# Kernel tuning notes

Measured on AMD Instinct MI355X. Metric: run time of the kernel, lower is better.

Reference implementation:

```python
import jax, jax.numpy as jnp
import numpy as np

NUM_HEADS = 8
BLOCK = 8      # block_size
HALO = 2       # kernel_size (halo width)


def _rel_to_abs(rel):
    # halo-style relative->absolute conversion
    # rel: [B, G, qh, qw, 2*p-1] -> [B, G, qh, qw, p]
    B, G, qh, qw, dim = rel.shape
    p = (dim + 1) // 2
    gap = p - qw
    flat = rel.reshape(B, G, qh, qw * dim)[:, :, :, qw - 1:-1]
    return flat.reshape(B, G, qh, qw, 2 * (p - 1))[:, :, :, :, gap:p + gap]


def _relative_logits(pos_q, pos_emb_h, pos_emb_w):
    # pos_q: [B, G, qb, qb, kd]; pos_emb_*: [kd, 2*p-1]
    rel_w = _rel_to_abs(jnp.einsum('bghwd,dr->bghwr', pos_q, pos_emb_w))  # [B,G,qb,qb,p] key-width
    q_t = pos_q.transpose(0, 1, 3, 2, 4)
    rel_h = _rel_to_abs(jnp.einsum('bgwhd,dr->bgwhr', q_t, pos_emb_h))
    rel_h = rel_h.transpose(0, 1, 3, 2, 4)  # [B,G,qb,qb,p] key-height
    return rel_h[..., :, None] + rel_w[..., None, :]  # [B,G,qb,qb,p,p]


def reference(x, w_q, w_kv, w_out, pos_emb_h, pos_emb_w):
    B, H, W, C = x.shape
    kd = C // NUM_HEADS                # per-head key dim
    kvk = BLOCK + 2 * HALO             # halo window size
    out_ch = w_out.shape[1]
    v_dim = out_ch // NUM_HEADS
    kv_per_head = (C + out_ch) // NUM_HEADS
    hh, ww = H // BLOCK, W // BLOCK
    scale = float(1.0 / np.sqrt(kd))

    # ---- query (1x1 conv == matmul), blockify ----
    q = (x @ w_q).reshape(B, hh, BLOCK, ww, BLOCK, NUM_HEADS, kd)
    q = q.transpose(0, 5, 1, 3, 2, 4, 6)  # [B,nh,hh,ww,qb,qb,kd]
    attn_q = q.reshape(B, NUM_HEADS, hh, ww, BLOCK * BLOCK, kd) * scale
    pos_q = q.reshape(B, NUM_HEADS * hh * ww, BLOCK, BLOCK, kd)

    # ---- key/value: 1x1 conv, halo pad, unfold into overlapping windows ----
    kv = jnp.pad(x @ w_kv, ((0, 0), (HALO, HALO), (HALO, HALO), (0, 0)))
    idx = np.arange(hh)[:, None] * BLOCK + np.arange(kvk)[None, :]  # [hh,kvk]
    idy = np.arange(ww)[:, None] * BLOCK + np.arange(kvk)[None, :]  # [ww,kvk]
    patches = kv[:, idx][:, :, :, idy]           # [B,hh,kvk,ww,kvk,kv_dim]
    patches = patches.transpose(0, 1, 3, 2, 4, 5)  # [B,hh,ww,kvk,kvk,kv_dim]
    kvh = patches.reshape(B, hh, ww, kvk, kvk, NUM_HEADS, kv_per_head)
    kvh = kvh.transpose(0, 5, 1, 2, 3, 4, 6).reshape(B, NUM_HEADS, hh, ww, kvk * kvk, kv_per_head)
    key, value = kvh[..., :kd], kvh[..., kd:]

    # ---- attention with relative position bias ----
    scores = jnp.einsum('bnhwqd,bnhwkd->bnhwqk', attn_q, key)
    pos = _relative_logits(pos_q, pos_emb_h, pos_emb_w)
    pos = pos.reshape(B, NUM_HEADS, hh, ww, BLOCK * BLOCK, kvk * kvk)
    attn = jax.nn.softmax(scores + pos, axis=-1)
    out = jnp.einsum('bnhwqk,bnhwkv->bnhwqv', attn, value)  # [B,nh,hh,ww,qb*qb,v_dim]

    # ---- de-blockify, output projection ----
    out = out.reshape(B, NUM_HEADS, hh, ww, BLOCK, BLOCK, v_dim)
    out = out.transpose(0, 2, 4, 3, 5, 1, 6).reshape(B, H, W, NUM_HEADS * v_dim)
    return out @ w_out


def setup_inputs() -> dict:
    key = jax.random.key(0)
    ks = jax.random.split(key, 6)
    B, H, W, C = 4, 128, 128, 256
    out_ch = 256
    kd = C // NUM_HEADS
    kvk = BLOCK + 2 * HALO
    std = kd ** -0.5
    return {
        'x': jax.random.normal(ks[0], (B, H, W, C), jnp.float32),
        'w_q': jax.random.normal(ks[1], (C, C), jnp.float32) * 0.02,
        'w_kv': jax.random.normal(ks[2], (C, C + out_ch), jnp.float32) * 0.02,
        'w_out': jax.random.normal(ks[3], (C, out_ch), jnp.float32) * 0.02,
        'pos_emb_h': jax.random.normal(ks[4], (kd, 2 * kvk - 1), jnp.float32) * std,
        'pos_emb_w': jax.random.normal(ks[5], (kd, 2 * kvk - 1), jnp.float32) * std,
    }
```

## Files before the change

kernel.cpp:

```cpp
#include <hip/hip_runtime.h>
#include <hip/hip_bf16.h>
#include <cstdint>


#define KVK 12
#define NKEYS 144
#define VT_S 160
#define PT_S 168
#define LOG2E 1.4426950408889634f

typedef unsigned int u32;
typedef unsigned short u16;
typedef __attribute__((ext_vector_type(8))) __bf16 bf16x8;
typedef __attribute__((ext_vector_type(4))) float f32x4;

__device__ __forceinline__ u16 f2bf(float f) {
    u32 x = __float_as_uint(f);
    return (u16)((x + 0x7fffu + ((x >> 16) & 1u)) >> 16);
}
__device__ __forceinline__ u32 cvtpk(float lo, float hi) {
    u32 d;
    asm("v_cvt_pk_bf16_f32 %0, %1, %2" : "=v"(d) : "v"(lo), "v"(hi));
    return d;
}
__device__ __forceinline__ float max3f(float a, float b, float c) {
    float d;
    asm("v_max3_f32 %0, %1, %2, %3" : "=v"(d) : "v"(a), "v"(b), "v"(c));
    return d;
}
__device__ __forceinline__ float exp2a(float x) {
    float d;
    asm("v_exp_f32 %0, %1" : "=v"(d) : "v"(x));
    return d;
}
__device__ __forceinline__ void gload16(const void* g, void* l) {
    __builtin_amdgcn_global_load_lds(
        (const __attribute__((address_space(1))) void*)g,
        (__attribute__((address_space(3))) void*)l, 16, 0, 0);
}

__global__ __launch_bounds__(256) void prep_weights(const float* __restrict__ wq,
                                                    const float* __restrict__ wkv,
                                                    const float* __restrict__ wout,
                                                    u16* __restrict__ wT,
                                                    u16* __restrict__ woutT,
                                                    const float* __restrict__ emb_h,
                                                    const float* __restrict__ emb_w,
                                                    u16* __restrict__ embT) {
    int blk = blockIdx.x, t = threadIdx.x;
    if (blk < 256) {
        int idx = blk * 256 + t; int nn = idx >> 8, k = idx & 255;
        wT[idx] = f2bf(wq[(long)k * 256 + nn]);
    } else if (blk < 768) {
        int idx = (blk - 256) * 256 + t; int nn = idx >> 8, k = idx & 255;
        float v = wkv[(long)k * 512 + nn];
        if ((nn & 32) == 0) v *= 0.2550348642f;
        wT[65536 + idx] = f2bf(v);
    } else if (blk < 1024) {
        int idx = (blk - 768) * 256 + t; int nn = idx >> 8, k = idx & 255;
        woutT[idx] = f2bf(wout[(long)k * 256 + nn]);
    } else if (blk == 1024) {
        for (int i = t; i < 736; i += 256) {
            int p = i >> 5, d = i & 31;
            embT[i] = f2bf(emb_h[d * 23 + p]);
        }
    } else {
        for (int i = t; i < 736; i += 256) {
            int p = i >> 5, d = i & 31;
            embT[736 + i] = f2bf(emb_w[d * 23 + p]);
        }
    }
}

__global__ __launch_bounds__(256) void gemm_qkv(const float* __restrict__ X,
                                                const u16* __restrict__ WT,
                                                u16* __restrict__ Qb,
                                                u16* __restrict__ KVb) {
    __shared__ u16 Apan[128 * 256];
    __shared__ u16 Bs[4096];
    const int t = threadIdx.x;
    const int w = t >> 6, lane = t & 63;
    const long m0 = (long)blockIdx.x * 128;
    const int wr = w >> 1, wc = w & 1;
    const int r = lane & 15, g = lane >> 4;

    #pragma unroll
    for (int i = 0; i < 16; ++i) {
        int v = i * 256 + t;
        int row = v >> 5, u = v & 31;
        const float* src = X + (m0 + row) * 256 + u * 8;
        float4 f0 = *reinterpret_cast<const float4*>(src);
        float4 f1 = *reinterpret_cast<const float4*>(src + 4);
        uint4 pk;
        pk.x = cvtpk(f0.x, f0.y); pk.y = cvtpk(f0.z, f0.w);
        pk.z = cvtpk(f1.x, f1.y); pk.w = cvtpk(f1.z, f1.w);
        *reinterpret_cast<uint4*>(&Apan[row * 256 + ((u ^ (row & 7)) << 3)]) = pk;
    }

    const int u0 = w * 128 + lane;
    const int rowB0 = u0 >> 2, csB0 = (u0 & 3) * 8;
    const int u1 = u0 + 64;
    const int rowB1 = u1 >> 2, csB1 = (u1 & 3) * 8;
    u16* BsW = &Bs[w * 1024];

    for (int nt = 0; nt < 6; ++nt) {
        const long n0 = nt * 128;
        const u16* Bg0 = WT + (n0 + rowB0) * 256 + csB0;
        const u16* Bg1 = WT + (n0 + rowB1) * 256 + csB1;

        f32x4 acc[4][4];
        #pragma unroll
        for (int i = 0; i < 4; ++i)
            #pragma unroll
            for (int j = 0; j < 4; ++j) acc[i][j] = (f32x4){0.f, 0.f, 0.f, 0.f};

        for (int k0 = 0; k0 < 256; k0 += 32) {
            gload16(Bg0 + k0, BsW);
            gload16(Bg1 + k0, BsW + 512);
            __syncthreads();
            bf16x8 a[4], b[4];
            const int cu = k0 >> 3;
            #pragma unroll
            for (int i = 0; i < 4; ++i) {
                int row = wr * 64 + i * 16 + r;
                a[i] = *reinterpret_cast<const bf16x8*>(
                    &Apan[row * 256 + (((cu + g) ^ (row & 7)) << 3)]);
            }
            #pragma unroll
            for (int j = 0; j < 4; ++j)
                b[j] = *reinterpret_cast<const bf16x8*>(&Bs[(wc * 64 + j * 16 + r) * 32 + g * 8]);
            #pragma unroll
            for (int i = 0; i < 4; ++i)
                #pragma unroll
                for (int j = 0; j < 4; ++j)
                    acc[i][j] = __builtin_amdgcn_mfma_f32_16x16x32_bf16(a[i], b[j], acc[i][j], 0, 0, 0);
            __syncthreads();
        }

        const bool isQ = (nt < 2);
        #pragma unroll
        for (int i = 0; i < 4; ++i) {
            #pragma unroll
            for (int j = 0; j < 4; ++j) {
                long col = n0 + wc * 64 + j * 16 + r;
                #pragma unroll
                for (int e = 0; e < 4; ++e) {
                    long row = m0 + wr * 64 + i * 16 + g * 4 + e;
                    u16 v = f2bf(acc[i][j][e]);
                    if (isQ) Qb[row * 256 + col] = v;
                    else     KVb[row * 512 + col - 256] = v;
                }
            }
        }
    }
}

__global__ __launch_bounds__(256) void mfma_gemm(const u16* __restrict__ A,
                                                 const u16* __restrict__ BT,
                                                 float* __restrict__ C, int N) {
    __shared__ u16 As[4096];
    __shared__ u16 Bs[4096];
    const int t = threadIdx.x;
    const int w = t >> 6, lane = t & 63;
    const long m0 = (long)blockIdx.x * 128;
    const long n0 = (long)blockIdx.y * 128;
    const int wr = w >> 1, wc = w & 1;
    const int r = lane & 15, g = lane >> 4;

    f32x4 acc[4][4];
    #pragma unroll
    for (int i = 0; i < 4; ++i)
        #pragma unroll
        for (int j = 0; j < 4; ++j) acc[i][j] = (f32x4){0.f, 0.f, 0.f, 0.f};

    const int u0 = w * 128 + lane;
    const int row0 = u0 >> 2, cs0 = (u0 & 3) * 8;
    const int u1 = u0 + 64;
    const int row1 = u1 >> 2, cs1 = (u1 & 3) * 8;
    const u16* Ag0 = A + (m0 + row0) * 256 + cs0;
    const u16* Ag1 = A + (m0 + row1) * 256 + cs1;
    const u16* Bg0 = BT + (n0 + row0) * 256 + cs0;
    const u16* Bg1 = BT + (n0 + row1) * 256 + cs1;
    u16* AsW = &As[w * 1024];
    u16* BsW = &Bs[w * 1024];

    for (int k0 = 0; k0 < 256; k0 += 32) {
        gload16(Ag0 + k0, AsW);
        gload16(Ag1 + k0, AsW + 512);
        gload16(Bg0 + k0, BsW);
        gload16(Bg1 + k0, BsW + 512);
        __syncthreads();
        bf16x8 a[4], b[4];
        #pragma unroll
        for (int i = 0; i < 4; ++i)
            a[i] = *reinterpret_cast<const bf16x8*>(&As[(wr * 64 + i * 16 + r) * 32 + g * 8]);
        #pragma unroll
        for (int j = 0; j < 4; ++j)
            b[j] = *reinterpret_cast<const bf16x8*>(&Bs[(wc * 64 + j * 16 + r) * 32 + g * 8]);
        #pragma unroll
        for (int i = 0; i < 4; ++i)
            #pragma unroll
            for (int j = 0; j < 4; ++j)
                acc[i][j] = __builtin_amdgcn_mfma_f32_16x16x32_bf16(a[i], b[j], acc[i][j], 0, 0, 0);
        __syncthreads();
    }

    #pragma unroll
    for (int i = 0; i < 4; ++i)
        #pragma unroll
        for (int j = 0; j < 4; ++j)
            #pragma unroll
            for (int e = 0; e < 4; ++e) {
                long row = m0 + wr * 64 + i * 16 + g * 4 + e;
                long col = n0 + wc * 64 + j * 16 + r;
                C[row * N + col] = acc[i][j][e];
            }
}

__global__ __launch_bounds__(256, 4) void attn_mfma(const u16* __restrict__ Qb,
                                                    const u16* __restrict__ KVb,
                                                    const u16* __restrict__ embT,
                                                    u16* __restrict__ Ob) {
    __shared__ __align__(16) char blob[26624];
    u16* Ks  = (u16*)blob;
    u16* Qe  = (u16*)(blob + 18432);
    u16* ehT = (u16*)(blob + 22528);
    u16* ewT = (u16*)(blob + 24576);
    u16* PT  = (u16*)blob;
    __shared__ u16 Vt[32 * VT_S];

    const int gblk = blockIdx.x;
    const int n = gblk & 7;
    const int bx = (gblk >> 3) & 15;
    const int by = (gblk >> 7) & 15;
    const int b = gblk >> 11;
    const int t = threadIdx.x;
    const int w = t >> 6, lane = t & 63;
    const int g = lane >> 4, r = lane & 15;

    const int q = w * 16 + r;
    const int qi = q >> 3, qj = q & 7;
    const long qrow = ((long)b * 128 + by * 8 + qi) * 128 + bx * 8 + qj;

    bf16x8 qa1 = *reinterpret_cast<const bf16x8*>(Qb + qrow * 256 + n * 32 + g * 8);

    for (int u = t; u < NKEYS * 8; u += 256) {
        int kk = u >> 3, part = u & 7;
        int ky = kk / KVK, kx = kk - ky * KVK;
        int gy = by * 8 + ky - 2, gx = bx * 8 + kx - 2;
        uint4 val = make_uint4(0u, 0u, 0u, 0u);
        if ((unsigned)gy < 128u && (unsigned)gx < 128u) {
            long row = ((long)b * 128 + gy) * 128 + gx;
            val = *reinterpret_cast<const uint4*>(KVb + row * 512 + n * 64 + part * 8);
        }
        if (part < 4) {
            int col = (part * 8) ^ ((kk & 7) << 3);
            *reinterpret_cast<uint4*>(&Ks[kk * 64 + col]) = val;
        } else {
            int d0 = (part - 4) * 8;
            u16 tmp[8];
            *reinterpret_cast<uint4*>(tmp) = val;
            #pragma unroll
            for (int i = 0; i < 8; ++i) {
                int d = d0 + i;
                Vt[d * VT_S + (kk ^ (((d >> 3) & 3) << 3))] = tmp[i];
            }
        }
    }
    for (int u = t; u < 576; u += 256) {
        int kk = u >> 2;
        int col = (32 + (u & 3) * 8) ^ ((kk & 7) << 3);
        *reinterpret_cast<uint4*>(&Ks[kk * 64 + col]) = make_uint4(0u, 0u, 0u, 0u);
    }
    if (t < 64) *reinterpret_cast<uint4*>(&Qe[t * 32 + 24]) = make_uint4(0u, 0u, 0u, 0u);
    if (t >= 224) {
        int d = t - 224;
        int sw = ((d >> 3) & 3) << 3;
        *reinterpret_cast<uint4*>(&Vt[d * VT_S + (144 ^ sw)]) = make_uint4(0u, 0u, 0u, 0u);
        *reinterpret_cast<uint4*>(&Vt[d * VT_S + (152 ^ sw)]) = make_uint4(0u, 0u, 0u, 0u);
    }
    if (t < 184) {
        uint4 v = *reinterpret_cast<const uint4*>(embT + t * 8);
        u16* dst = (t < 92) ? (ehT + t * 8) : (ewT + t * 8 - 736);
        *reinterpret_cast<uint4*>(dst) = v;
    }
    __syncthreads();

    {
        bf16x8 ah0 = *reinterpret_cast<const bf16x8*>(&ehT[r * 32 + g * 8]);
        bf16x8 ah1 = *reinterpret_cast<const bf16x8*>(&ehT[(16 + r) * 32 + g * 8]);
        bf16x8 aw0 = *reinterpret_cast<const bf16x8*>(&ewT[r * 32 + g * 8]);
        bf16x8 aw1 = *reinterpret_cast<const bf16x8*>(&ewT[(16 + r) * 32 + g * 8]);
        f32x4 z = (f32x4){0.f, 0.f, 0.f, 0.f};
        f32x4 rh0 = __builtin_amdgcn_mfma_f32_16x16x32_bf16(ah0, qa1, z, 0, 0, 0);
        f32x4 rh1 = __builtin_amdgcn_mfma_f32_16x16x32_bf16(ah1, qa1, z, 0, 0, 0);
        f32x4 rw0 = __builtin_amdgcn_mfma_f32_16x16x32_bf16(aw0, qa1, z, 0, 0, 0);
        f32x4 rw1 = __builtin_amdgcn_mfma_f32_16x16x32_bf16(aw1, qa1, z, 0, 0, 0);
        #pragma unroll
        for (int ti = 0; ti < 2; ++ti) {
            #pragma unroll
            for (int e = 0; e < 4; ++e) {
                int p = ti * 16 + g * 4 + e;
                float vh = (ti ? rh1[e] : rh0[e]) * LOG2E;
                float vw = (ti ? rw1[e] : rw0[e]) * LOG2E;
                int kyd = p + qi - 11;
                int kxd = p + qj - 11;
                if ((unsigned)kyd < 12u) Qe[q * 32 + kyd] = f2bf(vh);
                if ((unsigned)kxd < 12u) Qe[q * 32 + 12 + kxd] = f2bf(vw);
            }
        }
        if (t < NKEYS) {
            int ky = (t * 171) >> 11;
            int kx = t - 12 * ky;
            int sw = (t & 7) << 3;
            Ks[t * 64 + ((32 + ky) ^ sw)] = 0x3F80;
            Ks[t * 64 + ((44 + kx) ^ sw)] = 0x3F80;
        }
    }
    __syncthreads();

    bf16x8 qa2 = *reinterpret_cast<const bf16x8*>(&Qe[q * 32 + g * 8]);
    f32x4 acc[9];
    #pragma unroll
    for (int j = 0; j < 9; ++j) {
        int krow = j * 16 + r;
        int sw = (r & 7) << 3;
        bf16x8 kb0 = *reinterpret_cast<const bf16x8*>(&Ks[krow * 64 + ((g * 8) ^ sw)]);
        bf16x8 kb1 = *reinterpret_cast<const bf16x8*>(&Ks[krow * 64 + ((32 + g * 8) ^ sw)]);
        f32x4 z = (f32x4){0.f, 0.f, 0.f, 0.f};
        acc[j] = __builtin_amdgcn_mfma_f32_16x16x32_bf16(kb1, qa2,
                 __builtin_amdgcn_mfma_f32_16x16x32_bf16(kb0, qa1, z, 0, 0, 0), 0, 0, 0);
    }

    float mx = max3f(acc[0][0], acc[0][1], acc[0][2]);
    mx = fmaxf(mx, acc[0][3]);
    #pragma unroll
    for (int j = 1; j < 9; ++j)
        mx = max3f(mx, max3f(acc[j][0], acc[j][1], acc[j][2]), acc[j][3]);
    mx = fmaxf(mx, __shfl_xor(mx, 16));
    mx = fmaxf(mx, __shfl_xor(mx, 32));
    float s0 = 0.f, s1 = 0.f, s2 = 0.f, s3 = 0.f;
    u32 pkA[9], pkB[9];
    #pragma unroll
    for (int j = 0; j < 9; ++j) {
        float e0 = exp2a(acc[j][0] - mx);
        float e1 = exp2a(acc[j][1] - mx);
        float e2 = exp2a(acc[j][2] - mx);
        float e3 = exp2a(acc[j][3] - mx);
        s0 += e0; s1 += e1; s2 += e2; s3 += e3;
        pkA[j] = cvtpk(e0, e1);
        pkB[j] = cvtpk(e2, e3);
    }
    float sum = (s0 + s1) + (s2 + s3);
    sum += __shfl_xor(sum, 16);
    sum += __shfl_xor(sum, 32);
    const float inv = __builtin_amdgcn_rcpf(sum);

    __syncthreads();

    {
        const int ptb = q * PT_S;
        #pragma unroll
        for (int j = 0; j < 9; ++j) {
            *reinterpret_cast<u32*>(&PT[ptb + 16 * j + 4 * g]) = pkA[j];
            *reinterpret_cast<u32*>(&PT[ptb + 16 * j + 4 * g + 2]) = pkB[j];
        }
    }
    if (t < 64) {
        *reinterpret_cast<uint4*>(&PT[t * PT_S + 144]) = make_uint4(0u, 0u, 0u, 0u);
        *reinterpret_cast<uint4*>(&PT[t * PT_S + 152]) = make_uint4(0u, 0u, 0u, 0u);
    }
    __syncthreads();

    const int sw0 = (r >> 3) << 3;
    const int sw1 = (2 + (r >> 3)) << 3;
    f32x4 o0 = (f32x4){0.f, 0.f, 0.f, 0.f};
    f32x4 o1 = (f32x4){0.f, 0.f, 0.f, 0.f};
    #pragma unroll
    for (int kk = 0; kk < 5; ++kk) {
        bf16x8 pb = *reinterpret_cast<const bf16x8*>(&PT[q * PT_S + kk * 32 + g * 8]);
        bf16x8 va0 = *reinterpret_cast<const bf16x8*>(&Vt[r * VT_S + ((kk * 32 + g * 8) ^ sw0)]);
        bf16x8 va1 = *reinterpret_cast<const bf16x8*>(&Vt[(16 + r) * VT_S + ((kk * 32 + g * 8) ^ sw1)]);
        o0 = __builtin_amdgcn_mfma_f32_16x16x32_bf16(va0, pb, o0, 0, 0, 0);
        o1 = __builtin_amdgcn_mfma_f32_16x16x32_bf16(va1, pb, o1, 0, 0, 0);
    }
    {
        uint2 st0, st1;
        st0.x = cvtpk(o0[0] * inv, o0[1] * inv);
        st0.y = cvtpk(o0[2] * inv, o0[3] * inv);
        st1.x = cvtpk(o1[0] * inv, o1[1] * inv);
        st1.y = cvtpk(o1[2] * inv, o1[3] * inv);
        *reinterpret_cast<uint2*>(Ob + qrow * 256 + n * 32 + g * 4) = st0;
        *reinterpret_cast<uint2*>(Ob + qrow * 256 + n * 32 + 16 + g * 4) = st1;
    }
}

extern "C" void kernel_launch(void* const* d_in, const int* in_sizes, int n_in,
                              void* d_out, int out_size, void* d_ws, size_t ws_size,
                              hipStream_t stream) {
    const float* x     = (const float*)d_in[0];
    const float* w_q   = (const float*)d_in[1];
    const float* w_kv  = (const float*)d_in[2];
    const float* w_out = (const float*)d_in[3];
    const float* emb_h = (const float*)d_in[4];
    const float* emb_w = (const float*)d_in[5];

    u16* Qb = (u16*)d_out;
    char* ws = (char*)d_ws;
    u16* KVb   = (u16*)(ws);
    u16* Ob    = (u16*)(ws + (size_t)67108864);
    u16* wT    = (u16*)(ws + (size_t)100663296);
    u16* woutT = (u16*)(ws + (size_t)100663296 + 393216);
    u16* embT  = (u16*)(ws + (size_t)100663296 + 524288);

    dim3 blk(256);
    prep_weights<<<dim3(1026), blk, 0, stream>>>(w_q, w_kv, w_out, wT, woutT, emb_h, emb_w, embT);
    gemm_qkv<<<dim3(512), blk, 0, stream>>>(x, wT, Qb, KVb);
    attn_mfma<<<dim3(8192), blk, 0, stream>>>(Qb, KVb, embT, Ob);
    mfma_gemm<<<dim3(512, 2), blk, 0, stream>>>(Ob, woutT, (float*)d_out, 256);
}
```

Baseline: 141.1 us.

## Load QKV weights directly to registers and vectorize GEMM epilogue stores

The QKV projection GEMM stops staging weight tiles through shared memory and reads B fragments straight from global memory into registers. This removes the per-k-step barriers and fully unrolls the k loop. Both GEMMs swap the MFMA operand order so each lane holds four consecutive output columns of one row, which lets results go out as packed bf16 (uint2) or float4 stores instead of scalar stores. The cost is more global and L2 load traffic for the weights, with no shared-memory reuse across the waves that share columns.

```diff
diff --git a/kernel.cpp b/kernel.cpp
--- a/kernel.cpp
+++ b/kernel.cpp
@@ -77,7 +77,6 @@
                                                 u16* __restrict__ Qb,
                                                 u16* __restrict__ KVb) {
     __shared__ u16 Apan[128 * 256];
-    __shared__ u16 Bs[4096];
     const int t = threadIdx.x;
     const int w = t >> 6, lane = t & 63;
     const long m0 = (long)blockIdx.x * 128;
@@ -96,17 +95,14 @@
         pk.z = cvtpk(f1.x, f1.y); pk.w = cvtpk(f1.z, f1.w);
         *reinterpret_cast<uint4*>(&Apan[row * 256 + ((u ^ (row & 7)) << 3)]) = pk;
     }
-
-    const int u0 = w * 128 + lane;
-    const int rowB0 = u0 >> 2, csB0 = (u0 & 3) * 8;
-    const int u1 = u0 + 64;
-    const int rowB1 = u1 >> 2, csB1 = (u1 & 3) * 8;
-    u16* BsW = &Bs[w * 1024];
+    __syncthreads();
 
     for (int nt = 0; nt < 6; ++nt) {
-        const long n0 = nt * 128;
-        const u16* Bg0 = WT + (n0 + rowB0) * 256 + csB0;
-        const u16* Bg1 = WT + (n0 + rowB1) * 256 + csB1;
+        const long n0 = (long)nt * 128;
+        const u16* bp[4];
+        #pragma unroll
+        for (int j = 0; j < 4; ++j)
+            bp[j] = WT + (n0 + wc * 64 + j * 16 + r) * 256 + g * 8;
 
         f32x4 acc[4][4];
         #pragma unroll
@@ -114,11 +110,12 @@
             #pragma unroll
             for (int j = 0; j < 4; ++j) acc[i][j] = (f32x4){0.f, 0.f, 0.f, 0.f};
 
+        #pragma unroll
         for (int k0 = 0; k0 < 256; k0 += 32) {
-            gload16(Bg0 + k0, BsW);
-            gload16(Bg1 + k0, BsW + 512);
-            __syncthreads();
-            bf16x8 a[4], b[4];
+            bf16x8 b[4], a[4];
+            #pragma unroll
+            for (int j = 0; j < 4; ++j)
+                b[j] = *reinterpret_cast<const bf16x8*>(bp[j] + k0);
             const int cu = k0 >> 3;
             #pragma unroll
             for (int i = 0; i < 4; ++i) {
@@ -127,29 +124,24 @@
                     &Apan[row * 256 + (((cu + g) ^ (row & 7)) << 3)]);
             }
             #pragma unroll
-            for (int j = 0; j < 4; ++j)
-                b[j] = *reinterpret_cast<const bf16x8*>(&Bs[(wc * 64 + j * 16 + r) * 32 + g * 8]);
-            #pragma unroll
             for (int i = 0; i < 4; ++i)
                 #pragma unroll
                 for (int j = 0; j < 4; ++j)
-                    acc[i][j] = __builtin_amdgcn_mfma_f32_16x16x32_bf16(a[i], b[j], acc[i][j], 0, 0, 0);
-            __syncthreads();
+                    acc[i][j] = __builtin_amdgcn_mfma_f32_16x16x32_bf16(b[j], a[i], acc[i][j], 0, 0, 0);
         }
 
         const bool isQ = (nt < 2);
         #pragma unroll
         for (int i = 0; i < 4; ++i) {
+            long row = m0 + wr * 64 + i * 16 + r;
             #pragma unroll
             for (int j = 0; j < 4; ++j) {
-                long col = n0 + wc * 64 + j * 16 + r;
-                #pragma unroll
-                for (int e = 0; e < 4; ++e) {
-                    long row = m0 + wr * 64 + i * 16 + g * 4 + e;
-                    u16 v = f2bf(acc[i][j][e]);
-                    if (isQ) Qb[row * 256 + col] = v;
-                    else     KVb[row * 512 + col - 256] = v;
-                }
+                long colb = n0 + wc * 64 + j * 16 + g * 4;
+                uint2 st;
+                st.x = cvtpk(acc[i][j][0], acc[i][j][1]);
+                st.y = cvtpk(acc[i][j][2], acc[i][j][3]);
+                if (isQ) *reinterpret_cast<uint2*>(Qb + row * 256 + colb) = st;
+                else     *reinterpret_cast<uint2*>(KVb + row * 512 + colb - 256) = st;
             }
         }
     }
@@ -201,20 +193,20 @@
         for (int i = 0; i < 4; ++i)
             #pragma unroll
             for (int j = 0; j < 4; ++j)
-                acc[i][j] = __builtin_amdgcn_mfma_f32_16x16x32_bf16(a[i], b[j], acc[i][j], 0, 0, 0);
+                acc[i][j] = __builtin_amdgcn_mfma_f32_16x16x32_bf16(b[j], a[i], acc[i][j], 0, 0, 0);
         __syncthreads();
     }
 
     #pragma unroll
-    for (int i = 0; i < 4; ++i)
-        #pragma unroll
-        for (int j = 0; j < 4; ++j)
-            #pragma unroll
-            for (int e = 0; e < 4; ++e) {
-                long row = m0 + wr * 64 + i * 16 + g * 4 + e;
-                long col = n0 + wc * 64 + j * 16 + r;
-                C[row * N + col] = acc[i][j][e];
-            }
+    for (int i = 0; i < 4; ++i) {
+        long row = m0 + wr * 64 + i * 16 + r;
+        #pragma unroll
+        for (int j = 0; j < 4; ++j) {
+            long colb = n0 + wc * 64 + j * 16 + g * 4;
+            float4 st = make_float4(acc[i][j][0], acc[i][j][1], acc[i][j][2], acc[i][j][3]);
+            *reinterpret_cast<float4*>(C + row * N + colb) = st;
+        }
+    }
 }
 
 __global__ __launch_bounds__(256, 4) void attn_mfma(const u16* __restrict__ Qb,
```

New measurement: 173.4 us. 22.8% more time.
